# Optimization experiments

Hardware: AMD Instinct MI355X
Metric: run time of the kernel (lower is better)

The kernel has to match this reference:

```python
import jax, jax.numpy as jnp
import numpy as np

B, T, H, I, E = 2, 2048, 1024, 2048, 8
TOP_K = 2
RMS_EPS = 1e-6
ROUTING_GAIN = 1.0
INIT_STD = 0.02


def setup_inputs() -> dict:
    key = jax.random.key(0)
    ks = jax.random.split(key, 6)
    x = jax.random.normal(ks[0], (B, T, H), dtype=jnp.float32)
    q_norm_w = jnp.ones((H,), dtype=jnp.float32)
    k_proto = jax.random.normal(ks[1], (E, H), dtype=jnp.float32) * INIT_STD
    v_proto = jnp.eye(E, dtype=jnp.float32)  # nn.init.eye_
    gate_projs = jax.random.normal(ks[2], (E, H, I), dtype=jnp.float32) * INIT_STD
    up_projs = jax.random.normal(ks[3], (E, H, I), dtype=jnp.float32) * INIT_STD
    down_projs = jax.random.normal(ks[4], (E, I, H), dtype=jnp.float32) * INIT_STD
    return {"x": x, "q_norm_w": q_norm_w, "k_proto": k_proto, "v_proto": v_proto,
            "gate_projs": gate_projs, "up_projs": up_projs, "down_projs": down_projs}


def _routing_weights(x, q_norm_w, k_proto, v_proto):
    # CAPRRouter: RMSNorm -> proto attention -> softmax -> value mix -> gain
    q = x * jax.lax.rsqrt(jnp.mean(x * x, axis=-1, keepdims=True) + RMS_EPS) * q_norm_w
    attn = jax.nn.softmax(jnp.einsum('bth,ph->btp', q, k_proto) / np.sqrt(H).astype(np.float32), axis=-1)
    logits = jnp.einsum('btp,pq->btq', attn, v_proto) * ROUTING_GAIN
    rw = jax.nn.softmax(logits, axis=-1)  # [B,T,E]
    if TOP_K < E:
        tw, ti = jax.lax.top_k(rw, TOP_K)                       # [B,T,k]
        onehot = jax.nn.one_hot(ti, E, dtype=rw.dtype)          # [B,T,k,E]
        rw = jnp.einsum('btk,btke->bte', tw, onehot)            # scatter top-k back
        rw = rw / (jnp.sum(rw, axis=-1, keepdims=True) + 1e-9)
    return rw


def reference(x, q_norm_w, k_proto, v_proto, gate_projs, up_projs, down_projs):
    rw = _routing_weights(x, q_norm_w, k_proto, v_proto)  # [B,T,E]
    # Math-equivalent reassociation of torch's ('btp,phi->bthi' then 'bth,bthi->bti'):
    # per-expert GEMM then routing-weighted reduction over experts.
    gate_out = jnp.einsum('btp,btpi->bti', rw, jnp.einsum('bth,phi->btpi', x, gate_projs))
    up_out = jnp.einsum('btp,btpi->bti', rw, jnp.einsum('bth,phi->btpi', x, up_projs))
    intermediate = jax.nn.silu(gate_out) * up_out  # [B,T,I]
    output = jnp.einsum('btp,btph->bth', rw, jnp.einsum('bti,pih->btph', intermediate, down_projs))
    return output, rw
```

## Files before the change

kernel.cpp:

```cpp
#include <hip/hip_runtime.h>
#include <hip/hip_bf16.h>

#define NTOK 4096
#define HDIM 1024
#define IDIM 2048
#define NEXP 8
#define RBLK 16

typedef __attribute__((ext_vector_type(8))) short short8;
typedef __attribute__((ext_vector_type(4))) short short4b;
typedef __attribute__((ext_vector_type(4))) float f32x4;
typedef unsigned short ushort_t;

__device__ inline ushort_t f2bf(float f) {
    union { float f; unsigned u; } v; v.f = f;
    unsigned r = v.u + 0x7FFFu + ((v.u >> 16) & 1u);
    return (ushort_t)(r >> 16);
}
__device__ inline float bf2f(ushort_t h) {
    union { unsigned u; float f; } v; v.u = ((unsigned)h) << 16;
    return v.f;
}

#define GPTR(p) ((const __attribute__((address_space(1))) void*)(p))
#define LPTR(p) ((__attribute__((address_space(3))) void*)(p))

__global__ __launch_bounds__(256) void routing_kernel(
    const float* __restrict__ x, const float* __restrict__ qw,
    const float* __restrict__ kp, const float* __restrict__ vp,
    float* __restrict__ rw_out, int* __restrict__ counts,
    int* __restrict__ list, float2* __restrict__ topw,
    ushort_t* __restrict__ xb)
{
    __shared__ float kp_s[NEXP * HDIM];
    __shared__ float vp_s[NEXP * NEXP];
    __shared__ int lcnt[NEXP];
    __shared__ int base_s[NEXP];
    __shared__ int tinfo[RBLK][4];

    int tid = threadIdx.x;
    int wid = tid >> 6, lane = tid & 63;

    if (tid < NEXP) lcnt[tid] = 0;
    if (tid < NEXP * NEXP) vp_s[tid] = vp[tid];
    #pragma unroll
    for (int i = 0; i < 8; i++)
        ((float4*)kp_s)[tid + 256 * i] = ((const float4*)kp)[tid + 256 * i];

    float4 qv[4];
    #pragma unroll
    for (int j = 0; j < 4; j++) qv[j] = ((const float4*)qw)[lane + 64 * j];
    __syncthreads();

    for (int it = 0; it < RBLK / 4; it++) {
        int tl = wid * (RBLK / 4) + it;
        int t = blockIdx.x * RBLK + tl;
        const float4* xr4 = (const float4*)(x + (size_t)t * HDIM);
        float4 xv[4];
        #pragma unroll
        for (int j = 0; j < 4; j++) xv[j] = xr4[lane + 64 * j];

        ushort_t* xrow = xb + (size_t)t * HDIM;
        #pragma unroll
        for (int j = 0; j < 4; j++) {
            short4b o;
            o[0] = f2bf(xv[j].x); o[1] = f2bf(xv[j].y);
            o[2] = f2bf(xv[j].z); o[3] = f2bf(xv[j].w);
            ((short4b*)xrow)[lane + 64 * j] = o;
        }

        float ss = 0.f;
        #pragma unroll
        for (int j = 0; j < 4; j++)
            ss += xv[j].x*xv[j].x + xv[j].y*xv[j].y + xv[j].z*xv[j].z + xv[j].w*xv[j].w;
        #pragma unroll
        for (int off = 32; off; off >>= 1) ss += __shfl_xor(ss, off);
        float rms = rsqrtf(ss * (1.0f / HDIM) + 1e-6f);

        float4 q[4];
        #pragma unroll
        for (int j = 0; j < 4; j++) {
            q[j].x = xv[j].x * rms * qv[j].x; q[j].y = xv[j].y * rms * qv[j].y;
            q[j].z = xv[j].z * rms * qv[j].z; q[j].w = xv[j].w * rms * qv[j].w;
        }

        float d[NEXP];
        #pragma unroll
        for (int p = 0; p < NEXP; p++) {
            float acc = 0.f;
            #pragma unroll
            for (int j = 0; j < 4; j++) {
                float4 kv = ((const float4*)kp_s)[p * 256 + lane + 64 * j];
                acc += q[j].x*kv.x + q[j].y*kv.y + q[j].z*kv.z + q[j].w*kv.w;
            }
            #pragma unroll
            for (int off = 32; off; off >>= 1) acc += __shfl_xor(acc, off);
            d[p] = acc * (1.0f / 32.0f);
        }

        float m = d[0];
        #pragma unroll
        for (int p = 1; p < NEXP; p++) m = fmaxf(m, d[p]);
        float a[NEXP]; float s = 0.f;
        #pragma unroll
        for (int p = 0; p < NEXP; p++) { a[p] = expf(d[p] - m); s += a[p]; }
        float inv = 1.0f / s;
        #pragma unroll
        for (int p = 0; p < NEXP; p++) a[p] *= inv;
        float lg[NEXP];
        #pragma unroll
        for (int qi = 0; qi < NEXP; qi++) {
            float acc = 0.f;
            #pragma unroll
            for (int p = 0; p < NEXP; p++) acc += a[p] * vp_s[p * NEXP + qi];
            lg[qi] = acc;
        }
        float m2 = lg[0];
        #pragma unroll
        for (int p = 1; p < NEXP; p++) m2 = fmaxf(m2, lg[p]);
        float r[NEXP]; float s2 = 0.f;
        #pragma unroll
        for (int p = 0; p < NEXP; p++) { r[p] = expf(lg[p] - m2); s2 += r[p]; }
        float inv2 = 1.0f / s2;
        #pragma unroll
        for (int p = 0; p < NEXP; p++) r[p] *= inv2;
        int e0 = -1, e1 = -1; float w0 = -1.f, w1 = -1.f;
        #pragma unroll
        for (int p = 0; p < NEXP; p++) {
            if (r[p] > w0) { w1 = w0; e1 = e0; w0 = r[p]; e0 = p; }
            else if (r[p] > w1) { w1 = r[p]; e1 = p; }
        }
        float invn = 1.0f / (w0 + w1 + 1e-9f);
        float w0n = w0 * invn, w1n = w1 * invn;

        if (lane == 0) {
            #pragma unroll
            for (int p = 0; p < NEXP; p++)
                rw_out[(size_t)t * NEXP + p] = (p == e0) ? w0n : ((p == e1) ? w1n : 0.f);
            topw[t] = make_float2(w0n, w1n);
            int p0 = atomicAdd(&lcnt[e0], 1);
            int p1 = atomicAdd(&lcnt[e1], 1);
            tinfo[tl][0] = e0; tinfo[tl][1] = p0;
            tinfo[tl][2] = e1; tinfo[tl][3] = p1;
        }
    }
    __syncthreads();
    if (tid < NEXP) base_s[tid] = atomicAdd(&counts[tid], lcnt[tid]);
    __syncthreads();
    if (tid < RBLK) {
        int t = blockIdx.x * RBLK + tid;
        int e0 = tinfo[tid][0], p0 = tinfo[tid][1];
        int e1 = tinfo[tid][2], p1 = tinfo[tid][3];
        list[e0 * NTOK + base_s[e0] + p0] = t * 2;
        list[e1 * NTOK + base_s[e1] + p1] = t * 2 + 1;
    }
}

__global__ __launch_bounds__(256) void conv_t(const float* __restrict__ in, ushort_t* __restrict__ out,
                                              int K, int N) {
    __shared__ ushort_t ts[64][72];
    int e = blockIdx.z;
    int xb = blockIdx.x, yb = blockIdx.y;
    const float* ip = in + (size_t)e * K * N + (size_t)(yb * 64) * N + xb * 64;
    int NB = N / 128, KB = K / 64;
    int nb = xb >> 1, rhalf = (xb & 1) * 64;
    ushort_t* op = out + ((size_t)((size_t)e * NB + nb) * KB + yb) * (128 * 64);

    int tid = threadIdx.x;
    int r0 = tid >> 4;
    int c4 = (tid & 15) * 4;
    #pragma unroll
    for (int i = 0; i < 4; i++) {
        int r = r0 + i * 16;
        float4 v = *(const float4*)(ip + (size_t)r * N + c4);
        ts[c4+0][r] = f2bf(v.x); ts[c4+1][r] = f2bf(v.y);
        ts[c4+2][r] = f2bf(v.z); ts[c4+3][r] = f2bf(v.w);
    }
    __syncthreads();
    int n = tid >> 2;
    int kq = (tid & 3) * 16;
    int sw = (n & 7) << 3;
    short8 w0 = *(const short8*)&ts[n][kq];
    short8 w1 = *(const short8*)&ts[n][kq + 8];
    ushort_t* dst = op + (size_t)(rhalf + n) * 64;
    *(short8*)(dst + (kq ^ sw))       = w0;
    *(short8*)(dst + ((kq + 8) ^ sw)) = w1;
}

template<int KLEN, int KTOT, int FUSED, int OUTBF, int SPLITK>
__global__ __launch_bounds__(256) void gemm_bf16(
    const ushort_t* __restrict__ A,
    const ushort_t* __restrict__ W0, const ushort_t* __restrict__ W1,
    const int* __restrict__ counts, const int* __restrict__ list,
    void* __restrict__ out0, void* __restrict__ out1, int odim)
{
    constexpr int KB = KLEN / 64;
    constexpr int KBTOT = KTOT / 64;
    int zz = blockIdx.z;
    int e      = SPLITK ? (zz & (NEXP - 1)) : zz;
    int ksplit = SPLITK ? (zz >> 3) : 0;
    int koff   = ksplit * KLEN;

    int M = counts[e];
    int row0 = blockIdx.y * 128;
    if (row0 >= M) return;
    int nbTiles = odim / 128;
    int colb = blockIdx.x;
    const ushort_t* W = (FUSED && colb >= nbTiles) ? W1 : W0;
    void* outp        = (FUSED && colb >= nbTiles) ? out1 : out0;
    int nb = (FUSED && colb >= nbTiles) ? colb - nbTiles : colb;
    int col0 = nb * 128;

    __shared__ ushort_t smem[128 * 136];
    __shared__ int rowsS[128];
    ushort_t* Abuf = smem;
    ushort_t* Bbuf = smem + 8192;

    int tid = threadIdx.x;
    if (tid < 128) {
        int r = row0 + tid;
        rowsS[tid] = (r < M) ? list[e * NTOK + r] : -1;
    }
    __syncthreads();

    int wid = tid >> 6, lane = tid & 63;
    int wr = wid >> 1, wc = wid & 1;
    int la = lane & 15, lb = lane >> 4;

    int swu = ((((lane & 7) * 16) ^ ((lane >> 3) << 4)) >> 1);
    const ushort_t* aP[4];
    #pragma unroll
    for (int i = 0; i < 4; i++) {
        int r = (wid * 4 + i) * 8 + (lane >> 3);
        int ent = rowsS[r];
        int tok = (ent >= 0) ? (ent >> 1) : 0;
        aP[i] = A + (size_t)tok * KTOT + koff + swu;
    }
    const ushort_t* Wt = W + (size_t)((size_t)e * nbTiles + nb) * ((size_t)KBTOT * 8192)
                           + (size_t)(koff / 64) * 8192;

    int swr = (la & 7) << 3;
    int aoff[4][2], boff[4][2];
    #pragma unroll
    for (int m = 0; m < 4; m++)
        #pragma unroll
        for (int ks = 0; ks < 2; ks++)
            aoff[m][ks] = (wr * 64 + m * 16 + la) * 64 + ((ks * 32 + lb * 8) ^ swr);
    #pragma unroll
    for (int n = 0; n < 4; n++)
        #pragma unroll
        for (int ks = 0; ks < 2; ks++)
            boff[n][ks] = (wc * 64 + n * 16 + la) * 64 + ((ks * 32 + lb * 8) ^ swr);

    f32x4 acc[4][4];
    #pragma unroll
    for (int m = 0; m < 4; m++)
        #pragma unroll
        for (int n = 0; n < 4; n++) acc[m][n] = (f32x4){0.f, 0.f, 0.f, 0.f};

    for (int kt = 0; kt < KB; kt++) {
        #pragma unroll
        for (int i = 0; i < 4; i++) {
            int seg = wid * 4 + i;
            __builtin_amdgcn_global_load_lds(GPTR(aP[i] + kt * 64),
                                             LPTR(Abuf + seg * 512), 16, 0, 0);
            __builtin_amdgcn_global_load_lds(GPTR(Wt + (size_t)kt * 8192 + seg * 512 + lane * 8),
                                             LPTR(Bbuf + seg * 512), 16, 0, 0);
        }
        __syncthreads();
        #pragma unroll
        for (int ks = 0; ks < 2; ks++) {
            short8 af[4], bf[4];
            #pragma unroll
            for (int m = 0; m < 4; m++) af[m] = *(const short8*)&Abuf[aoff[m][ks]];
            #pragma unroll
            for (int n = 0; n < 4; n++) bf[n] = *(const short8*)&Bbuf[boff[n][ks]];
            #pragma unroll
            for (int m = 0; m < 4; m++)
                #pragma unroll
                for (int n = 0; n < 4; n++)
                    acc[m][n] = __builtin_amdgcn_mfma_f32_16x16x32_bf16(af[m], bf[n], acc[m][n], 0, 0, 0);
        }
        __syncthreads();
    }

    if (OUTBF) {
        ushort_t* ob = smem;
        #pragma unroll
        for (int m = 0; m < 4; m++)
            #pragma unroll
            for (int n = 0; n < 4; n++)
                #pragma unroll
                for (int j = 0; j < 4; j++)
                    ob[(wr * 64 + m * 16 + lb * 4 + j) * 136 + wc * 64 + n * 16 + la] =
                        f2bf(acc[m][n][j]);
        __syncthreads();
        int ch = tid & 15, rg = tid >> 4;
        #pragma unroll
        for (int i = 0; i < 8; i++) {
            int r = i * 16 + rg;
            int ent = rowsS[r];
            short8 v = *(const short8*)&ob[r * 136 + ch * 8];
            if (ent >= 0)
                *(short8*)((ushort_t*)outp + (size_t)ent * odim + col0 + ch * 8) = v;
        }
    } else {
        float* obF = (float*)smem;
        float* oF = (float*)outp + (size_t)ksplit * 2 * NTOK * odim;
        #pragma unroll
        for (int h = 0; h < 2; h++) {
            __syncthreads();
            if (wr == h) {
                #pragma unroll
                for (int m = 0; m < 4; m++)
                    #pragma unroll
                    for (int n = 0; n < 4; n++)
                        #pragma unroll
                        for (int j = 0; j < 4; j++)
                            obF[(m * 16 + lb * 4 + j) * 132 + wc * 64 + n * 16 + la] =
                                acc[m][n][j];
            }
            __syncthreads();
            int ch = tid & 31, rg = tid >> 5;
            #pragma unroll
            for (int i = 0; i < 8; i++) {
                int rl = i * 8 + rg;
                int ent = rowsS[h * 64 + rl];
                float4 v = *(const float4*)&obF[rl * 132 + ch * 4];
                if (ent >= 0)
                    *(float4*)(oF + (size_t)ent * odim + col0 + ch * 4) = v;
            }
        }
    }
}

__global__ __launch_bounds__(256) void silu_mix(
    const ushort_t* __restrict__ bg, const ushort_t* __restrict__ bu,
    const float2* __restrict__ topw, ushort_t* __restrict__ inter)
{
    int idx = blockIdx.x * 256 + threadIdx.x;
    int t = idx >> 8;
    int i8 = (idx & 255) * 8;
    float2 w = topw[t];
    short8 g0 = *(const short8*)(bg + (size_t)(2*t)   * IDIM + i8);
    short8 g1 = *(const short8*)(bg + (size_t)(2*t+1) * IDIM + i8);
    short8 u0 = *(const short8*)(bu + (size_t)(2*t)   * IDIM + i8);
    short8 u1 = *(const short8*)(bu + (size_t)(2*t+1) * IDIM + i8);
    short8 r;
    #pragma unroll
    for (int j = 0; j < 8; j++) {
        float g = w.x * bf2f((ushort_t)g0[j]) + w.y * bf2f((ushort_t)g1[j]);
        float u = w.x * bf2f((ushort_t)u0[j]) + w.y * bf2f((ushort_t)u1[j]);
        float s = g / (1.f + expf(-g)) * u;
        r[j] = f2bf(s);
    }
    *(short8*)(inter + (size_t)t * IDIM + i8) = r;
}

__global__ __launch_bounds__(256) void out_mix(
    const float* __restrict__ pout, const float2* __restrict__ topw,
    float* __restrict__ out)
{
    const size_t SPLITSZ = (size_t)2 * NTOK * HDIM;
    int idx = blockIdx.x * 256 + threadIdx.x;
    int t = idx >> 8;
    int h4 = (idx & 255) * 4;
    float2 w = topw[t];
    float4 a0 = *(const float4*)(pout + (size_t)(2*t)   * HDIM + h4);
    float4 b0 = *(const float4*)(pout + (size_t)(2*t+1) * HDIM + h4);
    float4 a1 = *(const float4*)(pout + SPLITSZ + (size_t)(2*t)   * HDIM + h4);
    float4 b1 = *(const float4*)(pout + SPLITSZ + (size_t)(2*t+1) * HDIM + h4);
    float4 r;
    r.x = w.x*(a0.x + a1.x) + w.y*(b0.x + b1.x);
    r.y = w.x*(a0.y + a1.y) + w.y*(b0.y + b1.y);
    r.z = w.x*(a0.z + a1.z) + w.y*(b0.z + b1.z);
    r.w = w.x*(a0.w + a1.w) + w.y*(b0.w + b1.w);
    *(float4*)(out + (size_t)t * HDIM + h4) = r;
}

extern "C" void kernel_launch(void* const* d_in, const int* in_sizes, int n_in,
                              void* d_out, int out_size, void* d_ws, size_t ws_size,
                              hipStream_t stream) {
    const float* x    = (const float*)d_in[0];
    const float* qw   = (const float*)d_in[1];
    const float* kp   = (const float*)d_in[2];
    const float* vp   = (const float*)d_in[3];
    const float* gate = (const float*)d_in[4];
    const float* up   = (const float*)d_in[5];
    const float* down = (const float*)d_in[6];
    float* out = (float*)d_out;
    float* rw_out = out + (size_t)NTOK * HDIM;

    char* ws = (char*)d_ws;
    int*      counts = (int*)ws;
    float2*   topw   = (float2*)(ws + 1024);
    int*      list   = (int*)(ws + 64 * 1024);
    ushort_t* xb     = (ushort_t*)(ws + 256 * 1024);
    ushort_t* wtg    = xb + (size_t)NTOK * HDIM;
    ushort_t* wtu    = wtg + (size_t)NEXP * HDIM * IDIM;
    ushort_t* wtd    = wtu + (size_t)NEXP * HDIM * IDIM;
    ushort_t* bg     = wtd + (size_t)NEXP * HDIM * IDIM;
    ushort_t* bu     = bg  + (size_t)2 * NTOK * IDIM;
    ushort_t* interb = bu  + (size_t)2 * NTOK * IDIM;
    float*    pout   = (float*)bg;

    hipMemsetAsync(counts, 0, NEXP * sizeof(int), stream);

    routing_kernel<<<NTOK / RBLK, 256, 0, stream>>>(x, qw, kp, vp, rw_out, counts, list, topw, xb);

    conv_t<<<dim3(IDIM / 64, HDIM / 64, NEXP), 256, 0, stream>>>(gate, wtg, HDIM, IDIM);
    conv_t<<<dim3(IDIM / 64, HDIM / 64, NEXP), 256, 0, stream>>>(up,   wtu, HDIM, IDIM);
    conv_t<<<dim3(HDIM / 64, IDIM / 64, NEXP), 256, 0, stream>>>(down, wtd, IDIM, HDIM);

    dim3 ggu(2 * IDIM / 128, NTOK / 128, NEXP);
    gemm_bf16<HDIM, HDIM, 1, 1, 0><<<ggu, 256, 0, stream>>>(xb, wtg, wtu, counts, list, bg, bu, IDIM);

    silu_mix<<<NTOK * IDIM / 8 / 256, 256, 0, stream>>>(bg, bu, topw, interb);

    dim3 gd(HDIM / 128, NTOK / 128, 2 * NEXP);
    gemm_bf16<IDIM / 2, IDIM, 0, 0, 1><<<gd, 256, 0, stream>>>(interb, wtd, (const ushort_t*)nullptr,
                                                               counts, list, pout, nullptr, HDIM);

    out_mix<<<NTOK * HDIM / 4 / 256, 256, 0, stream>>>(pout, topw, out);
}
```

Baseline: 277.3 us.

## Pack routed tokens contiguously per expert and drop split-K in down GEMM

Tokens are gathered per expert into a contiguous bf16 buffer, with a prefix-sum of expert counts, so the gate/up GEMM reads dense rows and writes outputs to compact expert slots instead of gathering through the routing list. The gate/up grid is remapped so that each XCD works on one expert, and silu_mix locates its inputs through per-token slot indices. The down GEMM drops split-K, which removes the second partial buffer and the extra reduction reads in out_mix. In exchange the change adds the pack_x and scan8 launches, and the down GEMM without split-K may expose fewer blocks.

```diff
diff --git a/kernel.cpp b/kernel.cpp
--- a/kernel.cpp
+++ b/kernel.cpp
@@ -30,7 +30,7 @@
     const float* __restrict__ kp, const float* __restrict__ vp,
     float* __restrict__ rw_out, int* __restrict__ counts,
     int* __restrict__ list, float2* __restrict__ topw,
-    ushort_t* __restrict__ xb)
+    int4* __restrict__ se)
 {
     __shared__ float kp_s[NEXP * HDIM];
     __shared__ float vp_s[NEXP * NEXP];
@@ -59,15 +59,6 @@
         float4 xv[4];
         #pragma unroll
         for (int j = 0; j < 4; j++) xv[j] = xr4[lane + 64 * j];
-
-        ushort_t* xrow = xb + (size_t)t * HDIM;
-        #pragma unroll
-        for (int j = 0; j < 4; j++) {
-            short4b o;
-            o[0] = f2bf(xv[j].x); o[1] = f2bf(xv[j].y);
-            o[2] = f2bf(xv[j].z); o[3] = f2bf(xv[j].w);
-            ((short4b*)xrow)[lane + 64 * j] = o;
-        }
 
         float ss = 0.f;
         #pragma unroll
@@ -149,11 +140,39 @@
     __syncthreads();
     if (tid < RBLK) {
         int t = blockIdx.x * RBLK + tid;
-        int e0 = tinfo[tid][0], p0 = tinfo[tid][1];
-        int e1 = tinfo[tid][2], p1 = tinfo[tid][3];
-        list[e0 * NTOK + base_s[e0] + p0] = t * 2;
-        list[e1 * NTOK + base_s[e1] + p1] = t * 2 + 1;
-    }
+        int e0 = tinfo[tid][0], p0 = base_s[tinfo[tid][0]] + tinfo[tid][1];
+        int e1 = tinfo[tid][2], p1 = base_s[tinfo[tid][2]] + tinfo[tid][3];
+        list[e0 * NTOK + p0] = t * 2;
+        list[e1 * NTOK + p1] = t * 2 + 1;
+        se[t] = make_int4(e0, p0, e1, p1);
+    }
+}
+
+__global__ void scan8(const int* __restrict__ counts, int* __restrict__ base) {
+    if (threadIdx.x == 0) {
+        int run = 0;
+        for (int e = 0; e < NEXP; e++) { base[e] = run; run += counts[e]; }
+    }
+}
+
+__global__ __launch_bounds__(256) void pack_x(
+    const float* __restrict__ x, const int* __restrict__ counts,
+    const int* __restrict__ base, const int* __restrict__ list,
+    ushort_t* __restrict__ xp)
+{
+    int e = blockIdx.y;
+    int M = counts[e];
+    int tid = threadIdx.x;
+    int p = blockIdx.x * 2 + (tid >> 7);
+    if (p >= M) return;
+    int tok = list[e * NTOK + p] >> 1;
+    int c = (tid & 127) * 8;
+    const float4* src = (const float4*)(x + (size_t)tok * HDIM + c);
+    float4 a = src[0], b = src[1];
+    short8 o;
+    o[0]=f2bf(a.x); o[1]=f2bf(a.y); o[2]=f2bf(a.z); o[3]=f2bf(a.w);
+    o[4]=f2bf(b.x); o[5]=f2bf(b.y); o[6]=f2bf(b.z); o[7]=f2bf(b.w);
+    *(short8*)(xp + (size_t)(base[e] + p) * HDIM + c) = o;
 }
 
 __global__ __launch_bounds__(256) void conv_t(const float* __restrict__ in, ushort_t* __restrict__ out,
@@ -187,57 +206,46 @@
     *(short8*)(dst + ((kq + 8) ^ sw)) = w1;
 }
 
-template<int KLEN, int KTOT, int FUSED, int OUTBF, int SPLITK>
-__global__ __launch_bounds__(256) void gemm_bf16(
-    const ushort_t* __restrict__ A,
-    const ushort_t* __restrict__ W0, const ushort_t* __restrict__ W1,
-    const int* __restrict__ counts, const int* __restrict__ list,
-    void* __restrict__ out0, void* __restrict__ out1, int odim)
+__global__ __launch_bounds__(256) void gemm_gu(
+    const ushort_t* __restrict__ xp,
+    const ushort_t* __restrict__ Wg, const ushort_t* __restrict__ Wu,
+    const int* __restrict__ counts, const int* __restrict__ base,
+    ushort_t* __restrict__ bg, ushort_t* __restrict__ bu)
 {
-    constexpr int KB = KLEN / 64;
-    constexpr int KBTOT = KTOT / 64;
-    int zz = blockIdx.z;
-    int e      = SPLITK ? (zz & (NEXP - 1)) : zz;
-    int ksplit = SPLITK ? (zz >> 3) : 0;
-    int koff   = ksplit * KLEN;
+    constexpr int K = HDIM, KB = K / 64, NBT = IDIM / 128;
+    int lin = blockIdx.x + 32 * blockIdx.y + 1024 * blockIdx.z;
+    int xcd = lin & 7;
+    int j = lin >> 3;
+    int rowbI = j & 31;
+    int colb = j >> 5;
+    int e = (xcd + ((colb & 1) << 2)) & 7;
 
     int M = counts[e];
-    int row0 = blockIdx.y * 128;
+    int row0 = rowbI * 128;
     if (row0 >= M) return;
-    int nbTiles = odim / 128;
-    int colb = blockIdx.x;
-    const ushort_t* W = (FUSED && colb >= nbTiles) ? W1 : W0;
-    void* outp        = (FUSED && colb >= nbTiles) ? out1 : out0;
-    int nb = (FUSED && colb >= nbTiles) ? colb - nbTiles : colb;
-    int col0 = nb * 128;
+    const ushort_t* W = (colb < NBT) ? Wg : Wu;
+    ushort_t* outp    = (colb < NBT) ? bg : bu;
+    int nb = (colb < NBT) ? colb : colb - NBT;
+    int slotbase = base[e] + row0;
 
     __shared__ ushort_t smem[128 * 136];
-    __shared__ int rowsS[128];
     ushort_t* Abuf = smem;
     ushort_t* Bbuf = smem + 8192;
 
     int tid = threadIdx.x;
-    if (tid < 128) {
-        int r = row0 + tid;
-        rowsS[tid] = (r < M) ? list[e * NTOK + r] : -1;
-    }
-    __syncthreads();
-
     int wid = tid >> 6, lane = tid & 63;
     int wr = wid >> 1, wc = wid & 1;
     int la = lane & 15, lb = lane >> 4;
 
-    int swu = ((((lane & 7) * 16) ^ ((lane >> 3) << 4)) >> 1);
+    int swu = (((lane & 7) ^ (lane >> 3)) * 8);
+    const ushort_t* Ax = xp + (size_t)slotbase * K;
     const ushort_t* aP[4];
     #pragma unroll
     for (int i = 0; i < 4; i++) {
         int r = (wid * 4 + i) * 8 + (lane >> 3);
-        int ent = rowsS[r];
-        int tok = (ent >= 0) ? (ent >> 1) : 0;
-        aP[i] = A + (size_t)tok * KTOT + koff + swu;
-    }
-    const ushort_t* Wt = W + (size_t)((size_t)e * nbTiles + nb) * ((size_t)KBTOT * 8192)
-                           + (size_t)(koff / 64) * 8192;
+        aP[i] = Ax + (size_t)r * K + swu;
+    }
+    const ushort_t* Wt = W + (size_t)((size_t)e * NBT + nb) * ((size_t)KB * 8192);
 
     int swr = (la & 7) << 3;
     int aoff[4][2], boff[4][2];
@@ -284,68 +292,42 @@
         __syncthreads();
     }
 
-    if (OUTBF) {
-        ushort_t* ob = smem;
-        #pragma unroll
-        for (int m = 0; m < 4; m++)
-            #pragma unroll
-            for (int n = 0; n < 4; n++)
-                #pragma unroll
-                for (int j = 0; j < 4; j++)
-                    ob[(wr * 64 + m * 16 + lb * 4 + j) * 136 + wc * 64 + n * 16 + la] =
-                        f2bf(acc[m][n][j]);
-        __syncthreads();
-        int ch = tid & 15, rg = tid >> 4;
-        #pragma unroll
-        for (int i = 0; i < 8; i++) {
-            int r = i * 16 + rg;
-            int ent = rowsS[r];
-            short8 v = *(const short8*)&ob[r * 136 + ch * 8];
-            if (ent >= 0)
-                *(short8*)((ushort_t*)outp + (size_t)ent * odim + col0 + ch * 8) = v;
-        }
-    } else {
-        float* obF = (float*)smem;
-        float* oF = (float*)outp + (size_t)ksplit * 2 * NTOK * odim;
-        #pragma unroll
-        for (int h = 0; h < 2; h++) {
-            __syncthreads();
-            if (wr == h) {
-                #pragma unroll
-                for (int m = 0; m < 4; m++)
-                    #pragma unroll
-                    for (int n = 0; n < 4; n++)
-                        #pragma unroll
-                        for (int j = 0; j < 4; j++)
-                            obF[(m * 16 + lb * 4 + j) * 132 + wc * 64 + n * 16 + la] =
-                                acc[m][n][j];
-            }
-            __syncthreads();
-            int ch = tid & 31, rg = tid >> 5;
-            #pragma unroll
-            for (int i = 0; i < 8; i++) {
-                int rl = i * 8 + rg;
-                int ent = rowsS[h * 64 + rl];
-                float4 v = *(const float4*)&obF[rl * 132 + ch * 4];
-                if (ent >= 0)
-                    *(float4*)(oF + (size_t)ent * odim + col0 + ch * 4) = v;
-            }
-        }
+    ushort_t* ob = smem;
+    #pragma unroll
+    for (int m = 0; m < 4; m++)
+        #pragma unroll
+        for (int n = 0; n < 4; n++)
+            #pragma unroll
+            for (int j2 = 0; j2 < 4; j2++)
+                ob[(wr * 64 + m * 16 + lb * 4 + j2) * 136 + wc * 64 + n * 16 + la] =
+                    f2bf(acc[m][n][j2]);
+    __syncthreads();
+    int ch = tid & 15, rg = tid >> 4;
+    #pragma unroll
+    for (int i = 0; i < 8; i++) {
+        int r = i * 16 + rg;
+        short8 v = *(const short8*)&ob[r * 136 + ch * 8];
+        if (row0 + r < M)
+            *(short8*)(outp + (size_t)(slotbase + r) * IDIM + nb * 128 + ch * 8) = v;
     }
 }
 
 __global__ __launch_bounds__(256) void silu_mix(
     const ushort_t* __restrict__ bg, const ushort_t* __restrict__ bu,
-    const float2* __restrict__ topw, ushort_t* __restrict__ inter)
+    const float2* __restrict__ topw, const int4* __restrict__ se,
+    const int* __restrict__ base, ushort_t* __restrict__ inter)
 {
     int idx = blockIdx.x * 256 + threadIdx.x;
     int t = idx >> 8;
     int i8 = (idx & 255) * 8;
     float2 w = topw[t];
-    short8 g0 = *(const short8*)(bg + (size_t)(2*t)   * IDIM + i8);
-    short8 g1 = *(const short8*)(bg + (size_t)(2*t+1) * IDIM + i8);
-    short8 u0 = *(const short8*)(bu + (size_t)(2*t)   * IDIM + i8);
-    short8 u1 = *(const short8*)(bu + (size_t)(2*t+1) * IDIM + i8);
+    int4 sv = se[t];
+    size_t s0 = ((size_t)base[sv.x] + sv.y) * IDIM + i8;
+    size_t s1 = ((size_t)base[sv.z] + sv.w) * IDIM + i8;
+    short8 g0 = *(const short8*)(bg + s0);
+    short8 g1 = *(const short8*)(bg + s1);
+    short8 u0 = *(const short8*)(bu + s0);
+    short8 u1 = *(const short8*)(bu + s1);
     short8 r;
     #pragma unroll
     for (int j = 0; j < 8; j++) {
@@ -357,24 +339,137 @@
     *(short8*)(inter + (size_t)t * IDIM + i8) = r;
 }
 
+__global__ __launch_bounds__(256) void gemm_dn(
+    const ushort_t* __restrict__ A, const ushort_t* __restrict__ W0,
+    const int* __restrict__ counts, const int* __restrict__ list,
+    float* __restrict__ pout)
+{
+    constexpr int K = IDIM, KB = K / 64, NBT = HDIM / 128;
+    int lin = blockIdx.x + 8 * blockIdx.y + 256 * blockIdx.z;
+    int e = lin & 7;
+    int j = lin >> 3;
+    int colb = j & 7;
+    int rowbI = j >> 3;
+
+    int M = counts[e];
+    int row0 = rowbI * 128;
+    if (row0 >= M) return;
+    int col0 = colb * 128;
+
+    __shared__ ushort_t smem[128 * 136];
+    __shared__ int rowsS[128];
+    ushort_t* Abuf = smem;
+    ushort_t* Bbuf = smem + 8192;
+
+    int tid = threadIdx.x;
+    if (tid < 128) {
+        int r = row0 + tid;
+        rowsS[tid] = (r < M) ? list[e * NTOK + r] : -1;
+    }
+    __syncthreads();
+
+    int wid = tid >> 6, lane = tid & 63;
+    int wr = wid >> 1, wc = wid & 1;
+    int la = lane & 15, lb = lane >> 4;
+
+    int swu = (((lane & 7) ^ (lane >> 3)) * 8);
+    const ushort_t* aP[4];
+    #pragma unroll
+    for (int i = 0; i < 4; i++) {
+        int r = (wid * 4 + i) * 8 + (lane >> 3);
+        int ent = rowsS[r];
+        int tok = (ent >= 0) ? (ent >> 1) : 0;
+        aP[i] = A + (size_t)tok * K + swu;
+    }
+    const ushort_t* Wt = W0 + (size_t)((size_t)e * NBT + colb) * ((size_t)KB * 8192);
+
+    int swr = (la & 7) << 3;
+    int aoff[4][2], boff[4][2];
+    #pragma unroll
+    for (int m = 0; m < 4; m++)
+        #pragma unroll
+        for (int ks = 0; ks < 2; ks++)
+            aoff[m][ks] = (wr * 64 + m * 16 + la) * 64 + ((ks * 32 + lb * 8) ^ swr);
+    #pragma unroll
+    for (int n = 0; n < 4; n++)
+        #pragma unroll
+        for (int ks = 0; ks < 2; ks++)
+            boff[n][ks] = (wc * 64 + n * 16 + la) * 64 + ((ks * 32 + lb * 8) ^ swr);
+
+    f32x4 acc[4][4];
+    #pragma unroll
+    for (int m = 0; m < 4; m++)
+        #pragma unroll
+        for (int n = 0; n < 4; n++) acc[m][n] = (f32x4){0.f, 0.f, 0.f, 0.f};
+
+    for (int kt = 0; kt < KB; kt++) {
+        #pragma unroll
+        for (int i = 0; i < 4; i++) {
+            int seg = wid * 4 + i;
+            __builtin_amdgcn_global_load_lds(GPTR(aP[i] + kt * 64),
+                                             LPTR(Abuf + seg * 512), 16, 0, 0);
+            __builtin_amdgcn_global_load_lds(GPTR(Wt + (size_t)kt * 8192 + seg * 512 + lane * 8),
+                                             LPTR(Bbuf + seg * 512), 16, 0, 0);
+        }
+        __syncthreads();
+        #pragma unroll
+        for (int ks = 0; ks < 2; ks++) {
+            short8 af[4], bf[4];
+            #pragma unroll
+            for (int m = 0; m < 4; m++) af[m] = *(const short8*)&Abuf[aoff[m][ks]];
+            #pragma unroll
+            for (int n = 0; n < 4; n++) bf[n] = *(const short8*)&Bbuf[boff[n][ks]];
+            #pragma unroll
+            for (int m = 0; m < 4; m++)
+                #pragma unroll
+                for (int n = 0; n < 4; n++)
+                    acc[m][n] = __builtin_amdgcn_mfma_f32_16x16x32_bf16(af[m], bf[n], acc[m][n], 0, 0, 0);
+        }
+        __syncthreads();
+    }
+
+    float* obF = (float*)smem;
+    #pragma unroll
+    for (int h = 0; h < 2; h++) {
+        __syncthreads();
+        if (wr == h) {
+            #pragma unroll
+            for (int m = 0; m < 4; m++)
+                #pragma unroll
+                for (int n = 0; n < 4; n++)
+                    #pragma unroll
+                    for (int j2 = 0; j2 < 4; j2++)
+                        obF[(m * 16 + lb * 4 + j2) * 132 + wc * 64 + n * 16 + la] =
+                            acc[m][n][j2];
+        }
+        __syncthreads();
+        int ch = tid & 31, rg = tid >> 5;
+        #pragma unroll
+        for (int i = 0; i < 8; i++) {
+            int rl = i * 8 + rg;
+            int ent = rowsS[h * 64 + rl];
+            float4 v = *(const float4*)&obF[rl * 132 + ch * 4];
+            if (ent >= 0)
+                *(float4*)(pout + (size_t)ent * HDIM + col0 + ch * 4) = v;
+        }
+    }
+}
+
 __global__ __launch_bounds__(256) void out_mix(
     const float* __restrict__ pout, const float2* __restrict__ topw,
     float* __restrict__ out)
 {
-    const size_t SPLITSZ = (size_t)2 * NTOK * HDIM;
     int idx = blockIdx.x * 256 + threadIdx.x;
     int t = idx >> 8;
     int h4 = (idx & 255) * 4;
     float2 w = topw[t];
-    float4 a0 = *(const float4*)(pout + (size_t)(2*t)   * HDIM + h4);
-    float4 b0 = *(const float4*)(pout + (size_t)(2*t+1) * HDIM + h4);
-    float4 a1 = *(const float4*)(pout + SPLITSZ + (size_t)(2*t)   * HDIM + h4);
-    float4 b1 = *(const float4*)(pout + SPLITSZ + (size_t)(2*t+1) * HDIM + h4);
+    float4 a = *(const float4*)(pout + (size_t)(2*t)   * HDIM + h4);
+    float4 b = *(const float4*)(pout + (size_t)(2*t+1) * HDIM + h4);
     float4 r;
-    r.x = w.x*(a0.x + a1.x) + w.y*(b0.x + b1.x);
-    r.y = w.x*(a0.y + a1.y) + w.y*(b0.y + b1.y);
-    r.z = w.x*(a0.z + a1.z) + w.y*(b0.z + b1.z);
-    r.w = w.x*(a0.w + a1.w) + w.y*(b0.w + b1.w);
+    r.x = w.x*a.x + w.y*b.x;
+    r.y = w.x*a.y + w.y*b.y;
+    r.z = w.x*a.z + w.y*b.z;
+    r.w = w.x*a.w + w.y*b.w;
     *(float4*)(out + (size_t)t * HDIM + h4) = r;
 }
 
@@ -393,10 +488,12 @@
 
     char* ws = (char*)d_ws;
     int*      counts = (int*)ws;
+    int*      basep  = (int*)(ws + 256);
     float2*   topw   = (float2*)(ws + 1024);
-    int*      list   = (int*)(ws + 64 * 1024);
-    ushort_t* xb     = (ushort_t*)(ws + 256 * 1024);
-    ushort_t* wtg    = xb + (size_t)NTOK * HDIM;
+    int4*     se     = (int4*)(ws + 64 * 1024);
+    int*      list   = (int*)(ws + 192 * 1024);
+    ushort_t* xp     = (ushort_t*)(ws + 512 * 1024);
+    ushort_t* wtg    = xp + (size_t)(NTOK * 2 + 128) * HDIM;
     ushort_t* wtu    = wtg + (size_t)NEXP * HDIM * IDIM;
     ushort_t* wtd    = wtu + (size_t)NEXP * HDIM * IDIM;
     ushort_t* bg     = wtd + (size_t)NEXP * HDIM * IDIM;
@@ -406,20 +503,22 @@
 
     hipMemsetAsync(counts, 0, NEXP * sizeof(int), stream);
 
-    routing_kernel<<<NTOK / RBLK, 256, 0, stream>>>(x, qw, kp, vp, rw_out, counts, list, topw, xb);
+    routing_kernel<<<NTOK / RBLK, 256, 0, stream>>>(x, qw, kp, vp, rw_out, counts, list, topw, se);
+    scan8<<<1, 64, 0, stream>>>(counts, basep);
 
     conv_t<<<dim3(IDIM / 64, HDIM / 64, NEXP), 256, 0, stream>>>(gate, wtg, HDIM, IDIM);
     conv_t<<<dim3(IDIM / 64, HDIM / 64, NEXP), 256, 0, stream>>>(up,   wtu, HDIM, IDIM);
     conv_t<<<dim3(HDIM / 64, IDIM / 64, NEXP), 256, 0, stream>>>(down, wtd, IDIM, HDIM);
 
-    dim3 ggu(2 * IDIM / 128, NTOK / 128, NEXP);
-    gemm_bf16<HDIM, HDIM, 1, 1, 0><<<ggu, 256, 0, stream>>>(xb, wtg, wtu, counts, list, bg, bu, IDIM);
-
-    silu_mix<<<NTOK * IDIM / 8 / 256, 256, 0, stream>>>(bg, bu, topw, interb);
-
-    dim3 gd(HDIM / 128, NTOK / 128, 2 * NEXP);
-    gemm_bf16<IDIM / 2, IDIM, 0, 0, 1><<<gd, 256, 0, stream>>>(interb, wtd, (const ushort_t*)nullptr,
-                                                               counts, list, pout, nullptr, HDIM);
+    pack_x<<<dim3(NTOK / 2, NEXP), 256, 0, stream>>>(x, counts, basep, list, xp);
+
+    dim3 ggu(32, 32, NEXP);
+    gemm_gu<<<ggu, 256, 0, stream>>>(xp, wtg, wtu, counts, basep, bg, bu);
+
+    silu_mix<<<NTOK * IDIM / 8 / 256, 256, 0, stream>>>(bg, bu, topw, se, basep, interb);
+
+    dim3 gd(8, 32, NEXP);
+    gemm_dn<<<gd, 256, 0, stream>>>(interb, wtd, counts, list, pout);
 
     out_mix<<<NTOK * HDIM / 4 / 256, 256, 0, stream>>>(pout, topw, out);
 }
```

Result: slower. 292.6 us (+5.5%).
